# Optimization experiments

Measured on AMD Instinct MI355X. Metric: run time of the kernel, lower is better.

## Reference

```python
import jax, jax.numpy as jnp
import numpy as np

B, IMG, P, CIN = 4, 384, 16, 3
G = IMG // P            # 24 patches per side
NP = G * G              # 576 patch tokens
N = NP + 1              # +cls
D, H, L, MLP, NC = 768, 12, 12, 3072, 1000
HD = D // H
SCALE = HD ** -0.5
NUM_REL = (2 * G - 1) * (2 * G - 1) + 3   # (2*1-1)*(2G-1)*(2G-1)+3 = 2212
EPS = 1e-6


def gen_rel_index():
    # window (1, G, G): depth diff is always 0, reduces to 2D BEiT indexing
    coords = np.stack(np.meshgrid(np.arange(G), np.arange(G), indexing='ij')).reshape(2, -1)
    rel = (coords[:, :, None] - coords[:, None, :]).transpose(1, 2, 0).copy()  # (NP,NP,2)
    rel[:, :, 0] += G - 1
    rel[:, :, 1] += G - 1
    rel[:, :, 0] *= 2 * G - 1
    idx = np.zeros((N, N), dtype=np.int32)
    idx[1:, 1:] = rel.sum(-1)
    idx[0, :] = NUM_REL - 3
    idx[:, 0] = NUM_REL - 2
    idx[0, 0] = NUM_REL - 1
    return jnp.asarray(idx)


def setup_inputs() -> dict:
    key = jax.random.key(0)
    ks = jax.random.split(key, 20)
    s = 0.02
    inp = {
        'x': jax.random.normal(ks[0], (B, CIN, IMG, IMG), jnp.float32),
        'patch_w': s * jax.random.normal(ks[1], (D, CIN * P * P), jnp.float32),
        'patch_b': jnp.zeros((D,), jnp.float32),
        'cls_token': s * jax.random.normal(ks[2], (1, 1, D), jnp.float32),
        'pos_embed': s * jax.random.normal(ks[3], (1, N, D), jnp.float32),
        'ln1_w': jnp.ones((L, D), jnp.float32),
        'ln1_b': jnp.zeros((L, D), jnp.float32),
        'qkv_w': s * jax.random.normal(ks[4], (L, 3 * D, D), jnp.float32),
        'q_bias': jnp.zeros((L, D), jnp.float32),
        'v_bias': jnp.zeros((L, D), jnp.float32),
        'proj_w': s * jax.random.normal(ks[5], (L, D, D), jnp.float32),
        'proj_b': jnp.zeros((L, D), jnp.float32),
        'ln2_w': jnp.ones((L, D), jnp.float32),
        'ln2_b': jnp.zeros((L, D), jnp.float32),
        'fc1_w': s * jax.random.normal(ks[6], (L, MLP, D), jnp.float32),
        'fc1_b': jnp.zeros((L, MLP), jnp.float32),
        'fc2_w': s * jax.random.normal(ks[7], (L, D, MLP), jnp.float32),
        'fc2_b': jnp.zeros((L, D), jnp.float32),
        'rel_table': s * jax.random.normal(ks[8], (L, NUM_REL, H), jnp.float32),
        'fc_norm_w': jnp.ones((D,), jnp.float32),
        'fc_norm_b': jnp.zeros((D,), jnp.float32),
        'head_w': s * jax.random.normal(ks[9], (NC, D), jnp.float32),
        'head_b': jnp.zeros((NC,), jnp.float32),
        'rel_index': gen_rel_index(),
    }
    return inp


def _ln(x, w, b):
    m = x.mean(-1, keepdims=True)
    v = ((x - m) ** 2).mean(-1, keepdims=True)
    return (x - m) * jax.lax.rsqrt(v + EPS) * w + b


def _beit_fwd(x, patch_w, patch_b, cls_token, pos_embed,
              ln1_w, ln1_b, qkv_w, q_bias, v_bias, proj_w, proj_b,
              ln2_w, ln2_b, fc1_w, fc1_b, fc2_w, fc2_b, rel_table,
              fc_norm_w, fc_norm_b, head_w, head_b, rel_index):
    # patch embed: conv P x P stride P == reshape + matmul; patch vec order (c, ph, pw)
    patches = x.reshape(B, CIN, G, P, G, P).transpose(0, 2, 4, 1, 3, 5).reshape(B, NP, CIN * P * P)
    tok = patches @ patch_w.T + patch_b                      # (B, NP, D)
    h = jnp.concatenate([jnp.broadcast_to(cls_token, (B, 1, D)), tok], axis=1) + pos_embed

    def block(h, p):
        l1w, l1b, qw, qb, vb, pw, pb, l2w, l2b, f1w, f1b, f2w, f2b, rt = p
        y = _ln(h, l1w, l1b)
        bias = jnp.concatenate([qb, jnp.zeros_like(qb), vb])  # k_bias frozen zeros
        qkv = (y @ qw.T + bias).reshape(B, N, 3, H, HD).transpose(2, 0, 3, 1, 4)
        q, k, v = qkv[0] * SCALE, qkv[1], qkv[2]              # (B,H,N,HD)
        attn = jnp.einsum('bhnd,bhmd->bhnm', q, k)
        rel = rt[rel_index].transpose(2, 0, 1)                # (H,N,N)
        attn = jax.nn.softmax(attn + rel[None], axis=-1)
        o = jnp.einsum('bhnm,bhmd->bhnd', attn, v).transpose(0, 2, 1, 3).reshape(B, N, D)
        h = h + (o @ pw.T + pb)
        y = _ln(h, l2w, l2b)
        y = jax.nn.gelu(y @ f1w.T + f1b, approximate=False) @ f2w.T + f2b
        return h + y, None

    xs = (ln1_w, ln1_b, qkv_w, q_bias, v_bias, proj_w, proj_b,
          ln2_w, ln2_b, fc1_w, fc1_b, fc2_w, fc2_b, rel_table)
    h, _ = jax.lax.scan(block, h, xs)

    pooled = h[:, 1:].mean(axis=1)                            # global_pool='avg' drops cls
    return _ln(pooled, fc_norm_w, fc_norm_b) @ head_w.T + head_b  # (B, NC)


def reference(x, patch_w, patch_b, cls_token, pos_embed,
              ln1_w, ln1_b, qkv_w, q_bias, v_bias, proj_w, proj_b,
              ln2_w, ln2_b, fc1_w, fc1_b, fc2_w, fc2_b, rel_table,
              fc_norm_w, fc_norm_b, head_w, head_b, rel_index):
    return _beit_fwd(x, patch_w, patch_b, cls_token, pos_embed,
                     ln1_w, ln1_b, qkv_w, q_bias, v_bias, proj_w, proj_b,
                     ln2_w, ln2_b, fc1_w, fc1_b, fc2_w, fc2_b, rel_table,
                     fc_norm_w, fc_norm_b, head_w, head_b, rel_index)
```

## Files before the change

kernel.cpp:

```cpp
#include <hip/hip_runtime.h>
#include <math.h>

typedef unsigned short u16;
typedef __bf16 bf16x8_t __attribute__((ext_vector_type(8)));
typedef u16 u16x8 __attribute__((ext_vector_type(8)));
typedef float f32x4 __attribute__((ext_vector_type(4)));

#define CBATCH 4
#define CN 577
#define CNP 576
#define CD 768
#define CH 12
#define CHD 64
#define CL 12
#define CMLP 3072
#define CVP 640
#define CROWS (CBATCH*CN)
#define CROWSP 2432
#define CNN2 332929
#define CBH (CBATCH*CH)
#define CSK 2
#define CMT 37

__device__ __forceinline__ float b2f(u16 u){
  unsigned x = ((unsigned)u) << 16;
  return __builtin_bit_cast(float, x);
}
__device__ __forceinline__ u16 f2b(float f){
  unsigned x = __builtin_bit_cast(unsigned, f);
  unsigned r = x + 0x7fffu + ((x >> 16) & 1u);
  return (u16)(r >> 16);
}

__device__ __forceinline__ f32x4 MFMA(u16x8 a, u16x8 b, f32x4 c){
  return __builtin_amdgcn_mfma_f32_16x16x32_bf16(
      __builtin_bit_cast(bf16x8_t, a), __builtin_bit_cast(bf16x8_t, b), c, 0, 0, 0);
}

__device__ __forceinline__ void gl_lds16(const u16* g, u16* l){
  __builtin_amdgcn_global_load_lds(
      (const __attribute__((address_space(1))) unsigned int*)g,
      (__attribute__((address_space(3))) unsigned int*)l, 16, 0, 0);
}


__global__ void cvt_kernel(const float* __restrict__ src, u16* __restrict__ dst, int n){
  int i = (blockIdx.x * 256 + threadIdx.x) * 4;
  if(i < n){
    float4 v = *reinterpret_cast<const float4*>(src + i);
    ushort4 o;
    o.x = f2b(v.x); o.y = f2b(v.y); o.z = f2b(v.z); o.w = f2b(v.w);
    *reinterpret_cast<ushort4*>(dst + i) = o;
  }
}

__global__ void zero_kernel(u16* __restrict__ p, int n){
  int i = (blockIdx.x * 256 + threadIdx.x) * 8;
  if(i < n){
    u16x8 z = {0,0,0,0,0,0,0,0};
    *reinterpret_cast<u16x8*>(p + i) = z;
  }
}

__global__ void im2col_kernel(const float* __restrict__ x, u16* __restrict__ out){
  int id = blockIdx.x * 256 + threadIdx.x;
  if(id >= 2304*768) return;
  int col = id % 768, row = id / 768;
  int b = row / 576, p = row % 576;
  int gy = p / 24, gx = p % 24;
  int c = col >> 8, rem = col & 255, py = rem >> 4, px = rem & 15;
  float v = x[(((long)(b*3 + c)*384) + gy*16 + py)*384 + gx*16 + px];
  out[id] = f2b(v);
}

__global__ void clspos_kernel(const float* __restrict__ cls, const float* __restrict__ pos,
                              float* __restrict__ h){
  int id = blockIdx.x * 256 + threadIdx.x;
  if(id < CBATCH*CD){
    int b = id / CD, d = id % CD;
    h[(long)b*CN*CD + d] = cls[d] + pos[d];
  }
}

template<bool BF16OUT>
__global__ void ln_kernel(const float* __restrict__ x, const float* __restrict__ w,
                          const float* __restrict__ bsh, u16* __restrict__ yb,
                          float* __restrict__ yf){
  int r = blockIdx.x;
  int tid = threadIdx.x;
  const float* px = x + (long)r*CD;
  float v0 = px[tid], v1 = px[tid+256], v2 = px[tid+512];
  __shared__ float red[4];
  float s = v0 + v1 + v2;
  #pragma unroll
  for(int m=1;m<64;m<<=1) s += __shfl_xor(s, m);
  if((tid & 63) == 0) red[tid>>6] = s;
  __syncthreads();
  s = red[0]+red[1]+red[2]+red[3];
  float mean = s * (1.0f/768.0f);
  float d0 = v0-mean, d1 = v1-mean, d2 = v2-mean;
  float s2 = d0*d0 + d1*d1 + d2*d2;
  __syncthreads();
  #pragma unroll
  for(int m=1;m<64;m<<=1) s2 += __shfl_xor(s2, m);
  if((tid & 63) == 0) red[tid>>6] = s2;
  __syncthreads();
  s2 = red[0]+red[1]+red[2]+red[3];
  float rs = rsqrtf(s2*(1.0f/768.0f) + 1e-6f);
  float o0 = d0*rs*w[tid]     + bsh[tid];
  float o1 = d1*rs*w[tid+256] + bsh[tid+256];
  float o2 = d2*rs*w[tid+512] + bsh[tid+512];
  if(BF16OUT){
    yb[(long)r*CD + tid]     = f2b(o0);
    yb[(long)r*CD + tid+256] = f2b(o1);
    yb[(long)r*CD + tid+512] = f2b(o2);
  } else {
    yf[(long)r*CD + tid]     = o0;
    yf[(long)r*CD + tid+256] = o1;
    yf[(long)r*CD + tid+512] = o2;
  }
}

template<bool DOLN>
__global__ void resid_ln_kernel(float* __restrict__ h, const float* __restrict__ part,
    const float* __restrict__ bias, const float* __restrict__ w,
    const float* __restrict__ bsh, u16* __restrict__ y){
  int r = blockIdx.x, tid = threadIdx.x;
  float v[3];
  #pragma unroll
  for(int j=0;j<3;j++){
    int c = tid + j*256;
    float t = h[(long)r*CD + c] + bias[c];
    #pragma unroll
    for(int sk=0; sk<CSK; sk++) t += part[((long)sk*CROWS + r)*CD + c];
    v[j] = t;
    h[(long)r*CD + c] = t;
  }
  if constexpr(DOLN){
    __shared__ float red[4];
    float s = v[0]+v[1]+v[2];
    #pragma unroll
    for(int m=1;m<64;m<<=1) s += __shfl_xor(s, m);
    if((tid & 63) == 0) red[tid>>6] = s;
    __syncthreads();
    s = red[0]+red[1]+red[2]+red[3];
    float mean = s * (1.0f/768.0f);
    float d0=v[0]-mean, d1=v[1]-mean, d2=v[2]-mean;
    float s2 = d0*d0+d1*d1+d2*d2;
    __syncthreads();
    #pragma unroll
    for(int m=1;m<64;m<<=1) s2 += __shfl_xor(s2, m);
    if((tid & 63) == 0) red[tid>>6] = s2;
    __syncthreads();
    s2 = red[0]+red[1]+red[2]+red[3];
    float rs = rsqrtf(s2*(1.0f/768.0f) + 1e-6f);
    y[(long)r*CD + tid]     = f2b(d0*rs*w[tid]     + bsh[tid]);
    y[(long)r*CD + tid+256] = f2b(d1*rs*w[tid+256] + bsh[tid+256]);
    y[(long)r*CD + tid+512] = f2b(d2*rs*w[tid+512] + bsh[tid+512]);
  }
}

__global__ void relbias_all_kernel(const int* __restrict__ ridx, const float* __restrict__ rtab,
                                   u16* __restrict__ attb){
  int id = blockIdx.x * 256 + threadIdx.x;
  if(id >= CNN2) return;
  int l = blockIdx.y;
  int idx = ridx[id];
  const float* rowp = rtab + (long)l*2212*12 + (long)idx*12;
  u16* dst = attb + (long)l*12*CNN2;
  #pragma unroll
  for(int hh=0; hh<12; hh++)
    dst[(long)hh*CNN2 + id] = f2b(rowp[hh]);
}

__global__ __launch_bounds__(256) void attn_kernel(
    const u16* __restrict__ q, const u16* __restrict__ k,
    const u16* __restrict__ vt, const u16* __restrict__ attb,
    u16* __restrict__ o_){
  __shared__ __align__(16) u16 lK[2][64*64];
  __shared__ __align__(16) u16 lV[2][64*64];
  __shared__ u16 pt[4][16*72];
  const int tid = threadIdx.x, lane = tid & 63, wv = tid >> 6;
  const int i15 = lane & 15, g4 = lane >> 4;
  const int qt = blockIdx.x, bh = blockIdx.y;
  const int b = bh / CH, hh = bh % CH;
  const int qrow0 = qt*64 + wv*16;
  const u16* qp = q + ((long)bh*CN + qrow0 + i15)*CHD + g4*8;
  u16x8 qa0 = *reinterpret_cast<const u16x8*>(qp);
  u16x8 qa1 = *reinterpret_cast<const u16x8*>(qp + 32);
  const u16* kbase = k + (long)bh*CN*CHD;
  const u16* vbase = vt + (long)bh*CHD*CVP;
  const u16* bb = attb + (long)hh*CNN2;

  const int srow = wv*16 + (lane>>3);
  const int scol = (lane&7)*8;
  const int sdst = wv*16*64;

  f32x4 po[4];
  float m[4], l[4];
  #pragma unroll
  for(int i=0;i<4;i++){ po[i]=(f32x4){0,0,0,0}; m[i]=-3.0e38f; l[i]=0.0f; }

  auto STAGE = [&](int t, int buf){
    const int kv0 = t*64;
    const u16* ks = kbase + ((long)(kv0 + srow))*CHD + scol;
    const u16* vs = vbase + ((long)srow)*CVP + kv0 + scol;
    gl_lds16(ks,          &lK[buf][sdst]);
    gl_lds16(ks + 8*CHD,  &lK[buf][sdst + 8*64]);
    gl_lds16(vs,          &lV[buf][sdst]);
    gl_lds16(vs + 8*CVP,  &lV[buf][sdst + 8*64]);
  };

  STAGE(0, 0);
  for(int t=0;t<10;t++){
    if(t+1 < 10){
      STAGE(t+1, (t+1)&1);
      asm volatile("s_waitcnt vmcnt(4)" ::: "memory");
    } else {
      asm volatile("s_waitcnt vmcnt(0)" ::: "memory");
    }
    __syncthreads();
    const int buf = t&1;
    const int kv0 = t*64;
    f32x4 sa[4];
    #pragma unroll
    for(int fc=0;fc<4;fc++){
      u16x8 k0 = *reinterpret_cast<const u16x8*>(&lK[buf][(fc*16+i15)*64 + g4*8]);
      u16x8 k1 = *reinterpret_cast<const u16x8*>(&lK[buf][(fc*16+i15)*64 + 32 + g4*8]);
      f32x4 z = (f32x4){0,0,0,0};
      z = MFMA(qa0, k0, z);
      z = MFMA(qa1, k1, z);
      sa[fc] = z;
    }
    float s[4][4];
    #pragma unroll
    for(int fc=0;fc<4;fc++){
      int kvc = kv0 + fc*16 + i15;
      bool valid = kvc < CN;
      #pragma unroll
      for(int r=0;r<4;r++){
        int qr = qrow0 + g4*4 + r;
        float bias = b2f(bb[(long)qr*CN + kvc]);
        s[fc][r] = valid ? (sa[fc][r] + bias) : -1e30f;
      }
    }
    float tm[4], ts[4], sc[4];
    #pragma unroll
    for(int r=0;r<4;r++)
      tm[r] = fmaxf(fmaxf(s[0][r],s[1][r]), fmaxf(s[2][r],s[3][r]));
    #pragma unroll
    for(int msk=1; msk<16; msk<<=1)
      #pragma unroll
      for(int r=0;r<4;r++)
        tm[r] = fmaxf(tm[r], __shfl_xor(tm[r], msk));
    #pragma unroll
    for(int r=0;r<4;r++){
      float mn = fmaxf(m[r], tm[r]);
      sc[r] = exp2f((m[r]-mn)*1.4426950408889634f);
      m[r] = mn;
      ts[r] = 0.f;
    }
    #pragma unroll
    for(int fc=0;fc<4;fc++)
      #pragma unroll
      for(int r=0;r<4;r++){
        float p = exp2f((s[fc][r]-m[r])*1.4426950408889634f);
        s[fc][r] = p; ts[r] += p;
      }
    #pragma unroll
    for(int msk=1; msk<16; msk<<=1)
      #pragma unroll
      for(int r=0;r<4;r++)
        ts[r] += __shfl_xor(ts[r], msk);
    #pragma unroll
    for(int r=0;r<4;r++) l[r] = l[r]*sc[r] + ts[r];
    #pragma unroll
    for(int d=0; d<4; d++)
      #pragma unroll
      for(int r=0;r<4;r++) po[d][r] *= sc[r];
    #pragma unroll
    for(int fc=0;fc<4;fc++)
      #pragma unroll
      for(int r=0;r<4;r++)
        pt[wv][(g4*4+r)*72 + fc*16 + i15] = f2b(s[fc][r]);
    u16x8 pa0 = *reinterpret_cast<const u16x8*>(&pt[wv][i15*72 + g4*8]);
    u16x8 pa1 = *reinterpret_cast<const u16x8*>(&pt[wv][i15*72 + 32 + g4*8]);
    #pragma unroll
    for(int d=0; d<4; d++){
      u16x8 v0 = *reinterpret_cast<const u16x8*>(&lV[buf][(d*16+i15)*64 + g4*8]);
      u16x8 v1 = *reinterpret_cast<const u16x8*>(&lV[buf][(d*16+i15)*64 + 32 + g4*8]);
      po[d] = MFMA(pa0, v0, po[d]);
      po[d] = MFMA(pa1, v1, po[d]);
    }
    __syncthreads();
  }
  #pragma unroll
  for(int d=0; d<4; d++)
    #pragma unroll
    for(int r=0;r<4;r++){
      int qr = qrow0 + g4*4 + r;
      if(qr < CN)
        o_[((long)(b*CN + qr))*CD + hh*CHD + d*16 + i15] = f2b(po[d][r] / l[r]);
    }
}

__global__ void pool_kernel(const float* __restrict__ h, float* __restrict__ pooled){
  int id = blockIdx.x * 256 + threadIdx.x;
  if(id >= CBATCH*CD) return;
  int b = id / CD, d = id % CD;
  const float* p = h + ((long)b*CN + 1)*CD + d;
  float s = 0.0f;
  for(int i=0;i<CNP;i++) s += p[(long)i*CD];
  pooled[id] = s * (1.0f/576.0f);
}

__global__ void head_kernel(const float* __restrict__ xn, const float* __restrict__ hw,
                            const float* __restrict__ hb, float* __restrict__ out){
  int nc = blockIdx.x;
  int tid = threadIdx.x;
  const float* wr = hw + (long)nc*CD;
  float w0 = wr[tid], w1 = wr[tid+256], w2 = wr[tid+512];
  __shared__ float red[4];
  for(int b=0;b<CBATCH;b++){
    const float* xr = xn + (long)b*CD;
    float s = w0*xr[tid] + w1*xr[tid+256] + w2*xr[tid+512];
    #pragma unroll
    for(int m=1;m<64;m<<=1) s += __shfl_xor(s, m);
    if((tid&63)==0) red[tid>>6] = s;
    __syncthreads();
    if(tid==0) out[b*1000 + nc] = red[0]+red[1]+red[2]+red[3] + hb[nc];
    __syncthreads();
  }
}


struct EpiArgs {
  float* hres;
  u16* outb;
  const float* bias;
  const float* pos;
  const float* qb;
  const float* vb;
  u16* q;
  u16* k;
  u16* vt;
  float* part;
};

enum { EPI_PATCH=0, EPI_QKV, EPI_GELU, EPI_PART };

template<int EPI>
__global__ __launch_bounds__(256,4) void gemm4(const u16* __restrict__ A, const u16* __restrict__ Bm,
    int M, int N, int K, int lda, int ldb, EpiArgs e){
  __shared__ __align__(16) u16 lA[3][64*32];
  __shared__ __align__(16) u16 lB[3][128*32];
  const int tid  = threadIdx.x;
  const int lane = tid & 63;
  const int wv   = tid >> 6;

  const int bm = blockIdx.y * 64, bn = blockIdx.x * 128;
  const int z  = blockIdx.z;
  A  += (long)z * K;
  Bm += (long)z * K;

  const int srow = wv*16 + (lane>>2);
  const u16* Asb = A  + (long)(bm + srow)*lda + (lane&3)*8;
  const u16* Bsb = Bm + (long)(bn + srow)*ldb + (lane&3)*8;
  const int ldst = wv*16*32;

  const int rbase = (wv>>1)*32;
  const int cbase = (wv&1)*64;
  const int i15 = lane & 15;
  const int k8off = (lane>>4)<<3;

  f32x4 acc[2][4];
  #pragma unroll
  for(int i=0;i<2;i++)
    #pragma unroll
    for(int j=0;j<4;j++)
      acc[i][j] = (f32x4){0.0f,0.0f,0.0f,0.0f};

  const int nkt = K >> 5;

  auto STAGE = [&](int kt, int slot){
    const u16* Ak = Asb + (long)kt*32;
    const u16* Bk = Bsb + (long)kt*32;
    gl_lds16(Ak,          &lA[slot][ldst]);
    gl_lds16(Bk,          &lB[slot][ldst]);
    gl_lds16(Bk + 64*ldb, &lB[slot][ldst + 64*32]);
  };

  STAGE(0, 0);
  if(nkt > 1) STAGE(1, 1);

  for(int kt=0; kt<nkt; kt++){
    if(kt+1 < nkt) asm volatile("s_waitcnt vmcnt(3) lgkmcnt(0)" ::: "memory");
    else           asm volatile("s_waitcnt vmcnt(0) lgkmcnt(0)" ::: "memory");
    __builtin_amdgcn_s_barrier();
    int nxt2 = kt + 2;
    if(nxt2 < nkt){ int sl = nxt2 % 3; STAGE(nxt2, sl); }
    const int cur = kt % 3;
    u16x8 af[2], bfr[4];
    #pragma unroll
    for(int f=0; f<2; f++)
      af[f]  = *reinterpret_cast<const u16x8*>(&lA[cur][(rbase + f*16 + i15)*32 + k8off]);
    #pragma unroll
    for(int f=0; f<4; f++)
      bfr[f] = *reinterpret_cast<const u16x8*>(&lB[cur][(cbase + f*16 + i15)*32 + k8off]);
    #pragma unroll
    for(int fr=0; fr<2; fr++)
      #pragma unroll
      for(int fc=0; fc<4; fc++)
        acc[fr][fc] = MFMA(af[fr], bfr[fc], acc[fr][fc]);
  }

  #pragma unroll
  for(int fr=0; fr<2; fr++){
    #pragma unroll
    for(int fc=0; fc<4; fc++){
      #pragma unroll
      for(int r=0;r<4;r++){
        int row = bm + rbase + fr*16 + ((lane>>4)<<2) + r;
        int col = bn + cbase + fc*16 + i15;
        if(row >= M || col >= N) continue;
        float v = acc[fr][fc][r];
        if constexpr(EPI == EPI_PATCH){
          int b = row/576, p = row%576;
          e.hres[((long)b*CN + 1 + p)*CD + col] = v + e.bias[col] + e.pos[(long)(1+p)*CD + col];
        } else if constexpr(EPI == EPI_QKV){
          int b = row/CN, n = row%CN;
          if(col < 768){
            int hh = col>>6, d = col&63;
            e.q[(((long)(b*CH+hh))*CN + n)*CHD + d] = f2b((v + e.qb[col]) * 0.125f);
          } else if(col < 1536){
            int c2 = col-768; int hh = c2>>6, d = c2&63;
            e.k[(((long)(b*CH+hh))*CN + n)*CHD + d] = f2b(v);
          } else {
            int c2 = col-1536; int hh = c2>>6, d = c2&63;
            e.vt[(((long)(b*CH+hh))*CHD + d)*CVP + n] = f2b(v + e.vb[c2]);
          }
        } else if constexpr(EPI == EPI_GELU){
          float t = v + e.bias[col];
          e.outb[(long)row*N + col] = f2b(t * 0.5f * (1.0f + erff(t*0.70710678118f)));
        } else {
          e.part[((long)z*CROWS + row)*CD + col] = v;
        }
      }
    }
  }
}


extern "C" void kernel_launch(void* const* d_in, const int* in_sizes, int n_in,
                              void* d_out, int out_size, void* d_ws, size_t ws_size,
                              hipStream_t stream){
  const float* x        = (const float*)d_in[0];
  const float* patch_w  = (const float*)d_in[1];
  const float* patch_b  = (const float*)d_in[2];
  const float* cls_tok  = (const float*)d_in[3];
  const float* pos_emb  = (const float*)d_in[4];
  const float* ln1_w    = (const float*)d_in[5];
  const float* ln1_b    = (const float*)d_in[6];
  const float* qkv_w    = (const float*)d_in[7];
  const float* q_bias   = (const float*)d_in[8];
  const float* v_bias   = (const float*)d_in[9];
  const float* proj_w   = (const float*)d_in[10];
  const float* proj_b   = (const float*)d_in[11];
  const float* ln2_w    = (const float*)d_in[12];
  const float* ln2_b    = (const float*)d_in[13];
  const float* fc1_w    = (const float*)d_in[14];
  const float* fc1_b    = (const float*)d_in[15];
  const float* fc2_w    = (const float*)d_in[16];
  const float* fc2_b    = (const float*)d_in[17];
  const float* rel_tab  = (const float*)d_in[18];
  const float* fcn_w    = (const float*)d_in[19];
  const float* fcn_b    = (const float*)d_in[20];
  const float* head_w   = (const float*)d_in[21];
  const float* head_b   = (const float*)d_in[22];
  const int*   rel_idx  = (const int*)d_in[23];
  float* out = (float*)d_out;
  char* ws = (char*)d_ws;

  size_t off = 0;
  auto alloc = [&](size_t bytes)->size_t{
    size_t o = off; off += (bytes + 255) & ~(size_t)255; return o;
  };
  const size_t OFF_H    = alloc((size_t)CROWS*CD*4);
  const size_t OFF_Y    = alloc((size_t)CROWSP*CD*2);
  const size_t OFF_Q    = alloc(((size_t)CBH*CN + 128)*CHD*2);
  const size_t OFF_K    = alloc(((size_t)CBH*CN + 128)*CHD*2);
  const size_t OFF_VT   = alloc((size_t)CBH*CHD*CVP*2);
  const size_t OFF_O    = alloc((size_t)CROWSP*CD*2);
  const size_t OFF_HID  = alloc((size_t)CROWSP*CMLP*2);
  const size_t OFF_PART = alloc((size_t)CSK*CROWS*CD*4);
  const size_t OFF_ATTB = alloc(((size_t)CL*CH*CNN2 + 64*1024)*2);
  const size_t OFF_WP0  = alloc((size_t)768*768*2);
  const size_t OFF_WQA  = alloc((size_t)CL*2304*768*2);
  const size_t OFF_WPA  = alloc((size_t)CL*768*768*2);
  const size_t OFF_W1A  = alloc((size_t)CL*3072*768*2);
  const size_t OFF_W2A  = alloc((size_t)CL*768*3072*2);
  const size_t OFF_PL   = alloc((size_t)CBATCH*CD*4);
  const size_t OFF_NM   = alloc((size_t)CBATCH*CD*4);
  (void)ws_size; (void)in_sizes; (void)n_in; (void)out_size;

  float* h      = (float*)(ws + OFF_H);
  u16*   y      = (u16*)(ws + OFF_Y);
  u16*   qb_    = (u16*)(ws + OFF_Q);
  u16*   kb_    = (u16*)(ws + OFF_K);
  u16*   vt_    = (u16*)(ws + OFF_VT);
  u16*   o_     = (u16*)(ws + OFF_O);
  u16*   hid    = (u16*)(ws + OFF_HID);
  float* part   = (float*)(ws + OFF_PART);
  u16*   attb   = (u16*)(ws + OFF_ATTB);
  u16*   wp0    = (u16*)(ws + OFF_WP0);
  u16*   wqA    = (u16*)(ws + OFF_WQA);
  u16*   wpA    = (u16*)(ws + OFF_WPA);
  u16*   w1A    = (u16*)(ws + OFF_W1A);
  u16*   w2A    = (u16*)(ws + OFF_W2A);
  float* pooled = (float*)(ws + OFF_PL);
  float* normed = (float*)(ws + OFF_NM);

  auto cvt = [&](const float* src, u16* dst, long n){
    cvt_kernel<<<dim3((unsigned)((n/4 + 255)/256)), dim3(256), 0, stream>>>(src, dst, (int)n);
  };

  {
    int n = CBH*CHD*CVP;
    zero_kernel<<<dim3((n/8 + 255)/256), dim3(256), 0, stream>>>(vt_, n);
  }
  im2col_kernel<<<dim3((2304*768 + 255)/256), dim3(256), 0, stream>>>(x, hid);
  cvt(patch_w, wp0, 768*768);
  cvt(qkv_w,  wqA, (long)CL*2304*768);
  cvt(proj_w, wpA, (long)CL*768*768);
  cvt(fc1_w,  w1A, (long)CL*3072*768);
  cvt(fc2_w,  w2A, (long)CL*768*3072);
  relbias_all_kernel<<<dim3((CNN2 + 255)/256, CL), dim3(256), 0, stream>>>(
      rel_idx, rel_tab, attb);

  {
    EpiArgs e{}; e.hres = h; e.bias = patch_b; e.pos = pos_emb;
    gemm4<EPI_PATCH><<<dim3(6,36,1), dim3(256), 0, stream>>>(
        hid, wp0, 2304, 768, 768, 768, 768, e);
  }
  clspos_kernel<<<dim3(12), dim3(256), 0, stream>>>(cls_tok, pos_emb, h);

  ln_kernel<true><<<dim3(CROWS), dim3(256), 0, stream>>>(
      h, ln1_w, ln1_b, y, nullptr);

  for(int l=0; l<CL; l++){
    {
      EpiArgs e{}; e.qb = q_bias + l*CD; e.vb = v_bias + l*CD;
      e.q = qb_; e.k = kb_; e.vt = vt_;
      gemm4<EPI_QKV><<<dim3(18,CMT,1), dim3(256), 0, stream>>>(
          y, wqA + (long)l*2304*768, CROWS, 2304, 768, 768, 768, e);
    }
    attn_kernel<<<dim3(10, CBH), dim3(256), 0, stream>>>(
        qb_, kb_, vt_, attb + (long)l*CH*CNN2, o_);
    {
      EpiArgs e{}; e.part = part;
      gemm4<EPI_PART><<<dim3(6,CMT,CSK), dim3(256), 0, stream>>>(
          o_, wpA + (long)l*768*768, CROWS, 768, 768/CSK, 768, 768, e);
    }
    resid_ln_kernel<true><<<dim3(CROWS), dim3(256), 0, stream>>>(
        h, part, proj_b + l*CD, ln2_w + l*CD, ln2_b + l*CD, y);
    {
      EpiArgs e{}; e.outb = hid; e.bias = fc1_b + l*CMLP;
      gemm4<EPI_GELU><<<dim3(24,CMT,1), dim3(256), 0, stream>>>(
          y, w1A + (long)l*3072*768, CROWS, 3072, 768, 768, 768, e);
    }
    {
      EpiArgs e{}; e.part = part;
      gemm4<EPI_PART><<<dim3(6,CMT,CSK), dim3(256), 0, stream>>>(
          hid, w2A + (long)l*768*3072, CROWS, 768, 3072/CSK, 3072, 3072, e);
    }
    if(l+1 < CL){
      resid_ln_kernel<true><<<dim3(CROWS), dim3(256), 0, stream>>>(
          h, part, fc2_b + l*CD, ln1_w + (l+1)*CD, ln1_b + (l+1)*CD, y);
    } else {
      resid_ln_kernel<false><<<dim3(CROWS), dim3(256), 0, stream>>>(
          h, part, fc2_b + l*CD, nullptr, nullptr, nullptr);
    }
  }

  pool_kernel<<<dim3(12), dim3(256), 0, stream>>>(h, pooled);
  ln_kernel<false><<<dim3(CBATCH), dim3(256), 0, stream>>>(
      pooled, fcn_w, fcn_b, nullptr, normed);
  head_kernel<<<dim3(1000), dim3(256), 0, stream>>>(normed, head_w, head_b, out);
}
```

Baseline: 2.097 ms.

## Remap workgroups to XCD-contiguous chunks and raise fc2 split-K to four

Adds an XCD-aware block index remap so that consecutive logical tiles in GEMMs and attention land on the same XCD, which is meant to improve L2 reuse of shared A/B tiles and K/V data on the 8-XCD MI355X. GEMM tiles are now walked column-major (bn outer, bm inner) within each XCD chunk. Separately, the fc2 GEMM split-K goes from 2 to 4 to give a small grid more parallelism. In exchange the residual kernel reads more partial buffers and the workspace grows.

```diff
diff --git a/kernel.cpp b/kernel.cpp
--- a/kernel.cpp
+++ b/kernel.cpp
@@ -19,7 +19,8 @@
 #define CROWSP 2432
 #define CNN2 332929
 #define CBH (CBATCH*CH)
-#define CSK 2
+#define CSKP 2
+#define CSKF 4
 #define CMT 37
 
 __device__ __forceinline__ float b2f(u16 u){
@@ -41,6 +42,12 @@
   __builtin_amdgcn_global_load_lds(
       (const __attribute__((address_space(1))) unsigned int*)g,
       (__attribute__((address_space(3))) unsigned int*)l, 16, 0, 0);
+}
+
+__device__ __forceinline__ int xcd_chunk(int o, int nwg){
+  int q8 = nwg >> 3, r8 = nwg & 7;
+  int xcd = o & 7, sl = o >> 3;
+  return (xcd < r8 ? xcd*(q8+1) : r8*(q8+1) + (xcd - r8)*q8) + sl;
 }
 
 
@@ -121,7 +128,7 @@
   }
 }
 
-template<bool DOLN>
+template<bool DOLN, int NSK>
 __global__ void resid_ln_kernel(float* __restrict__ h, const float* __restrict__ part,
     const float* __restrict__ bias, const float* __restrict__ w,
     const float* __restrict__ bsh, u16* __restrict__ y){
@@ -132,7 +139,7 @@
     int c = tid + j*256;
     float t = h[(long)r*CD + c] + bias[c];
     #pragma unroll
-    for(int sk=0; sk<CSK; sk++) t += part[((long)sk*CROWS + r)*CD + c];
+    for(int sk=0; sk<NSK; sk++) t += part[((long)sk*CROWS + r)*CD + c];
     v[j] = t;
     h[(long)r*CD + c] = t;
   }
@@ -182,7 +189,9 @@
   __shared__ u16 pt[4][16*72];
   const int tid = threadIdx.x, lane = tid & 63, wv = tid >> 6;
   const int i15 = lane & 15, g4 = lane >> 4;
-  const int qt = blockIdx.x, bh = blockIdx.y;
+  const int o = blockIdx.y * 10 + blockIdx.x;
+  const int cm = xcd_chunk(o, 480);
+  const int bh = cm / 10, qt = cm % 10;
   const int b = bh / CH, hh = bh % CH;
   const int qrow0 = qt*64 + wv*16;
   const u16* qp = q + ((long)bh*CN + qrow0 + i15)*CHD + g4*8;
@@ -358,7 +367,12 @@
   const int lane = tid & 63;
   const int wv   = tid >> 6;
 
-  const int bm = blockIdx.y * 64, bn = blockIdx.x * 128;
+  const int gx = gridDim.x, gy = gridDim.y;
+  const int o = blockIdx.y * gx + blockIdx.x;
+  const int cm = xcd_chunk(o, gx*gy);
+  const int bn = (cm / gy) * 128;
+  const int bm = (cm % gy) * 64;
+
   const int z  = blockIdx.z;
   A  += (long)z * K;
   Bm += (long)z * K;
@@ -492,7 +506,7 @@
   const size_t OFF_VT   = alloc((size_t)CBH*CHD*CVP*2);
   const size_t OFF_O    = alloc((size_t)CROWSP*CD*2);
   const size_t OFF_HID  = alloc((size_t)CROWSP*CMLP*2);
-  const size_t OFF_PART = alloc((size_t)CSK*CROWS*CD*4);
+  const size_t OFF_PART = alloc((size_t)CSKF*CROWS*CD*4);
   const size_t OFF_ATTB = alloc(((size_t)CL*CH*CNN2 + 64*1024)*2);
   const size_t OFF_WP0  = alloc((size_t)768*768*2);
   const size_t OFF_WQA  = alloc((size_t)CL*2304*768*2);
@@ -558,10 +572,10 @@
         qb_, kb_, vt_, attb + (long)l*CH*CNN2, o_);
     {
       EpiArgs e{}; e.part = part;
-      gemm4<EPI_PART><<<dim3(6,CMT,CSK), dim3(256), 0, stream>>>(
-          o_, wpA + (long)l*768*768, CROWS, 768, 768/CSK, 768, 768, e);
-    }
-    resid_ln_kernel<true><<<dim3(CROWS), dim3(256), 0, stream>>>(
+      gemm4<EPI_PART><<<dim3(6,CMT,CSKP), dim3(256), 0, stream>>>(
+          o_, wpA + (long)l*768*768, CROWS, 768, 768/CSKP, 768, 768, e);
+    }
+    resid_ln_kernel<true,CSKP><<<dim3(CROWS), dim3(256), 0, stream>>>(
         h, part, proj_b + l*CD, ln2_w + l*CD, ln2_b + l*CD, y);
     {
       EpiArgs e{}; e.outb = hid; e.bias = fc1_b + l*CMLP;
@@ -570,14 +584,14 @@
     }
     {
       EpiArgs e{}; e.part = part;
-      gemm4<EPI_PART><<<dim3(6,CMT,CSK), dim3(256), 0, stream>>>(
-          hid, w2A + (long)l*768*3072, CROWS, 768, 3072/CSK, 3072, 3072, e);
+      gemm4<EPI_PART><<<dim3(6,CMT,CSKF), dim3(256), 0, stream>>>(
+          hid, w2A + (long)l*768*3072, CROWS, 768, 3072/CSKF, 3072, 3072, e);
     }
     if(l+1 < CL){
-      resid_ln_kernel<true><<<dim3(CROWS), dim3(256), 0, stream>>>(
+      resid_ln_kernel<true,CSKF><<<dim3(CROWS), dim3(256), 0, stream>>>(
           h, part, fc2_b + l*CD, ln1_w + (l+1)*CD, ln1_b + (l+1)*CD, y);
     } else {
-      resid_ln_kernel<false><<<dim3(CROWS), dim3(256), 0, stream>>>(
+      resid_ln_kernel<false,CSKF><<<dim3(CROWS), dim3(256), 0, stream>>>(
           h, part, fc2_b + l*CD, nullptr, nullptr, nullptr);
     }
   }
```

Measured after the change: 2.087 ms. Within noise of the previous version (-0.5%).
